# Performance work log

Measured on AMD Instinct MI355X. Metric: run time of the kernel, lower is better.

## Reference

```python
import itertools
import jax, jax.numpy as jnp
import numpy as np

RES = 14
B = 64
DIM = 384
NH = 8
KD = 32
DV = 128  # attn_ratio * key_dim
SCALE = KD ** -0.5


def _bias_idxs(res):
    points = list(itertools.product(range(res), range(res)))
    offs, idxs = {}, []
    for p1 in points:
        for p2 in points:
            o = (abs(p1[0] - p2[0]), abs(p1[1] - p2[1]))
            if o not in offs:
                offs[o] = len(offs)
            idxs.append(offs[o])
    n = res * res
    return np.asarray(idxs, dtype=np.int32).reshape(n, n), len(offs)


def setup_inputs() -> dict:
    key = jax.random.key(0)
    ks = jax.random.split(key, 16)
    idxs, n_off = _bias_idxs(RES)  # n_off == 196 for res=14
    f = lambda k, shape, s=0.05: jax.random.normal(k, shape, dtype=jnp.float32) * s
    return {
        "x": jax.random.normal(ks[0], (B, DIM, RES, RES), dtype=jnp.float32),
        "qw": f(ks[1], (NH * KD, DIM)), "qb": f(ks[2], (NH * KD,)),
        "kw": f(ks[3], (NH * KD, DIM)), "kb": f(ks[4], (NH * KD,)),
        "vw": f(ks[5], (NH * DV, DIM)), "vb": f(ks[6], (NH * DV,)),
        "vlw": f(ks[7], (NH * DV, 1, 3, 3)), "vlb": f(ks[8], (NH * DV,)),
        "th1_w": f(ks[9], (NH, NH), 0.3), "th1_b": f(ks[10], (NH,)),
        "th2_w": f(ks[11], (NH, NH), 0.3), "th2_b": f(ks[12], (NH,)),
        "projw": f(ks[13], (DIM, NH * DV)), "projb": f(ks[14], (DIM,)),
        "bias_seg": f(ks[15], (NH, n_off), 0.5),
        "bias_idxs": jnp.asarray(idxs),
    }


def reference(x, qw, qb, kw, kb, vw, vb, vlw, vlb,
              th1_w, th1_b, th2_w, th2_b, projw, projb,
              bias_seg, bias_idxs):
    Bb, C, H, W = x.shape
    N = H * W
    xf = x.reshape(Bb, C, N)
    # 1x1 conv (+ folded BN) projections
    q = (jnp.einsum('oc,bcn->bon', qw, xf) + qb[:, None]).reshape(Bb, NH, KD, N).transpose(0, 1, 3, 2)  # [B,h,N,kd]
    k = (jnp.einsum('oc,bcn->bon', kw, xf) + kb[:, None]).reshape(Bb, NH, KD, N)                        # [B,h,kd,N]
    v4 = (jnp.einsum('oc,bcn->bon', vw, xf) + vb[:, None]).reshape(Bb, NH * DV, H, W)
    # depthwise 3x3 local branch (+ folded BN)
    v_local = jax.lax.conv_general_dilated(
        v4, vlw, window_strides=(1, 1), padding=[(1, 1), (1, 1)],
        dimension_numbers=('NCHW', 'OIHW', 'NCHW'), feature_group_count=NH * DV,
    ) + vlb[None, :, None, None]
    v = v4.reshape(Bb, NH, DV, N).transpose(0, 1, 3, 2)  # [B,h,N,dv]
    # attention scores + relative bias (bicubic interp 196->196 is identity)
    attn = jnp.einsum('bhnk,bhkm->bhnm', q, k) * SCALE
    bias = bias_seg[:, bias_idxs]  # [h,N,N]
    attn = attn + bias[None]
    # talking heads (1x1 conv over head dim) -> softmax -> talking heads
    attn = jnp.einsum('hg,bgnm->bhnm', th1_w, attn) + th1_b[None, :, None, None]
    attn = jax.nn.softmax(attn, axis=-1)
    attn = jnp.einsum('hg,bgnm->bhnm', th2_w, attn) + th2_b[None, :, None, None]
    o = jnp.einsum('bhnm,bhmd->bhnd', attn, v)           # [B,h,N,dv]
    o = o.transpose(0, 1, 3, 2).reshape(Bb, NH * DV, H, W) + v_local
    # proj: ReLU -> 1x1 conv (+ folded BN)
    o = jax.nn.relu(o)
    out = jnp.einsum('oc,bchw->bohw', projw, o) + projb[None, :, None, None]
    return out
```

## Files before the change

### kernel.cpp

```cpp
#include <hip/hip_runtime.h>
#include <hip/hip_bf16.h>


#define RES   14
#define NSP   196
#define NHD   8
#define KDIM  32
#define DVV   128
#define DIM   384
#define NQK   256
#define SCALE 0.17677669529663687f
#define SROW  224
#define NSTRIP 13

typedef __attribute__((ext_vector_type(8))) short bf16x8;
typedef __attribute__((ext_vector_type(4))) float f32x4;
typedef unsigned short u16;
typedef unsigned int u32;

__device__ __forceinline__ u16 f2b(float f) {
    union { __hip_bfloat16 b; u16 u; } c; c.b = __float2bfloat16(f); return c.u;
}
__device__ __forceinline__ float b2f(u16 u) {
    union { __hip_bfloat16 b; u16 u; } c; c.u = u; return __bfloat162float(c.b);
}

__device__ __forceinline__ void gld16(const void* g, void* l) {
    __builtin_amdgcn_global_load_lds(
        (__attribute__((address_space(1))) void*)(unsigned long long)(const char*)g,
        (__attribute__((address_space(3))) void*)l, 16, 0, 0);
}

__device__ __forceinline__ void gemm128_bk64(const char* Aseg, long rbA,
                                             const char* Bseg, long rbB, int kIters,
                                             u16* A_lds, u16* B_lds, f32x4 acc[4][4])
{
    const int tid  = threadIdx.x;
    const int wid  = tid >> 6;
    const int lane = tid & 63;
    const int lrow = lane >> 2;
    const int lcb  = (lane & 3) << 4;
    const int r0   = wid * 32;
    const int wm   = (wid & 1) * 64, wn = (wid >> 1) * 64;
    const int l15  = lane & 15, lq8 = (lane >> 4) * 8;

    #pragma unroll
    for (int i = 0; i < 4; ++i)
        #pragma unroll
        for (int j = 0; j < 4; ++j) acc[i][j] = (f32x4){0.f, 0.f, 0.f, 0.f};

    const char* ap0 = Aseg + (long)(r0 + lrow) * rbA + lcb;
    const char* ap1 = ap0 + 16 * rbA;
    const char* bp0 = Bseg + (long)(r0 + lrow) * rbB + lcb;
    const char* bp1 = bp0 + 16 * rbB;
    u16* la0 = A_lds + r0 * 32;
    u16* la1 = la0 + 512;
    u16* lb0 = B_lds + r0 * 32;
    u16* lb1 = lb0 + 512;

    for (int kk = 0; kk < kIters; ++kk) {
        gld16(ap0, la0);        gld16(ap1, la1);
        gld16(bp0, lb0);        gld16(bp1, lb1);
        gld16(ap0 + 64, la0 + 4096); gld16(ap1 + 64, la1 + 4096);
        gld16(bp0 + 64, lb0 + 4096); gld16(bp1 + 64, lb1 + 4096);
        ap0 += 128; ap1 += 128; bp0 += 128; bp1 += 128;
        __syncthreads();
        #pragma unroll
        for (int s = 0; s < 2; ++s) {
            bf16x8 af[4], bfr[4];
            #pragma unroll
            for (int i = 0; i < 4; ++i)
                af[i] = *(const bf16x8*)&A_lds[s * 4096 + (wm + i * 16 + l15) * 32 + lq8];
            #pragma unroll
            for (int j = 0; j < 4; ++j)
                bfr[j] = *(const bf16x8*)&B_lds[s * 4096 + (wn + j * 16 + l15) * 32 + lq8];
            #pragma unroll
            for (int i = 0; i < 4; ++i)
                #pragma unroll
                for (int j = 0; j < 4; ++j)
                    acc[i][j] = __builtin_amdgcn_mfma_f32_16x16x32_bf16(
                        af[i], bfr[j], acc[i][j], 0, 0, 0);
        }
        __syncthreads();
    }
}

__global__ __launch_bounds__(256) void k_prep(
    const float* __restrict__ qw, const float* __restrict__ kw,
    const float* __restrict__ vw, const float* __restrict__ pw,
    const float* __restrict__ th1w, const float* __restrict__ th1b,
    const float* __restrict__ bias_seg, const float* __restrict__ vlw,
    const float* __restrict__ x,
    u16* __restrict__ wqkv, u16* __restrict__ pwb, float* __restrict__ biasmix,
    u16* __restrict__ wpack, u16* __restrict__ xb)
{
    __shared__ float t[32][33];
    const int bid = blockIdx.x;
    if (bid < 3883) {
        int i = bid * 256 + threadIdx.x;
        if (i < 98304)       wqkv[i] = f2b(qw[i]);
        else if (i < 196608) wqkv[i] = f2b(kw[i - 98304]);
        else if (i < 589824) wqkv[i] = f2b(vw[i - 196608]);
        else if (i < 983040) pwb[i - 589824] = f2b(pw[i - 589824]);
        else if (i < 984608) {
            int i2 = i - 983040;
            int hh = i2 / NSP, off = i2 - hh * NSP;
            float a = th1b[hh];
            #pragma unroll
            for (int g = 0; g < 8; ++g) a += th1w[hh * 8 + g] * bias_seg[g * NSP + off];
            biasmix[i2] = a;
        } else if (i < 993824) {
            int i2 = i - 984608;
            int g = i2 / 72, r = i2 - g * 72;
            int tap = r >> 3, tt = r & 7;
            wpack[i2] = f2b(vlw[(g * 8 + tt) * 9 + tap]);
        }
    } else {
        const int L = bid - 3883;
        const int b = L / 84, r = L - b * 84;
        const int c0 = (r / 7) * 32, n0 = (r % 7) * 32;
        const int tx = threadIdx.x & 31, ty = threadIdx.x >> 5;
        #pragma unroll
        for (int l = 0; l < 4; ++l) {
            int c = c0 + ty + 8 * l, n = n0 + tx;
            t[ty + 8 * l][tx] = (n < NSP) ? x[((long)b * DIM + c) * NSP + n] : 0.f;
        }
        __syncthreads();
        #pragma unroll
        for (int l = 0; l < 4; ++l) {
            int n = n0 + ty + 8 * l, c = c0 + tx;
            if (n < NSP) xb[((long)b * NSP + n) * DIM + c] = f2b(t[tx][ty + 8 * l]);
        }
    }
}

__global__ __launch_bounds__(256) void k_qkv(
    const u16* __restrict__ xb, const u16* __restrict__ wqkv,
    const float* __restrict__ qb, const float* __restrict__ kb,
    const float* __restrict__ vb,
    u16* __restrict__ qt, u16* __restrict__ kb16, u16* __restrict__ vt)
{
    __shared__ u16 A_lds[8192], B_lds[8192];
    const int m0 = blockIdx.x * 128, oc0 = blockIdx.y * 128;
    f32x4 acc[4][4];
    gemm128_bk64((const char*)xb + (long)m0 * 768, 768,
                 (const char*)wqkv + (long)oc0 * 768, 768, 6, A_lds, B_lds, acc);

    const int tid = threadIdx.x, wid = tid >> 6, lane = tid & 63;
    const int wm = (wid & 1) * 64, wn = (wid >> 1) * 64;
    const int col = lane & 15, quad = lane >> 4;
    #pragma unroll
    for (int i = 0; i < 4; ++i) {
        #pragma unroll
        for (int j = 0; j < 4; ++j) {
            #pragma unroll
            for (int r = 0; r < 4; ++r) {
                int m  = m0 + wm + i * 16 + quad * 4 + r;
                int oc = oc0 + wn + j * 16 + col;
                int b = m / NSP, n = m - b * NSP;
                float v = acc[i][j][r];
                if (oc < 256) {
                    qt[(long)m * NQK + oc] = f2b(v + qb[oc]);
                } else if (oc < 512) {
                    int o = oc - 256;
                    kb16[(long)m * NQK + o] = f2b(v + kb[o]);
                } else {
                    int o = oc - 512, h = o >> 7, d = o & 127;
                    vt[(((long)b * NHD + h) * NSP + n) * DVV + d] = f2b(v + vb[o]);
                }
            }
        }
    }
}

__global__ __launch_bounds__(256) void k_vtT(
    const u16* __restrict__ vt, u16* __restrict__ vtT)
{
    __shared__ u16 t[32][33];
    const int bh = blockIdx.z, d0 = blockIdx.y * 32, n0 = blockIdx.x * 32;
    const int tx = threadIdx.x & 31, ty = threadIdx.x >> 5;
    #pragma unroll
    for (int l = 0; l < 4; ++l) {
        int n = n0 + ty + 8 * l, d = d0 + tx;
        t[ty + 8 * l][tx] = (n < NSP) ? vt[((long)bh * NSP + n) * DVV + d] : (u16)0;
    }
    __syncthreads();
    #pragma unroll
    for (int l = 0; l < 4; ++l) {
        int d = d0 + ty + 8 * l, m = n0 + tx;
        vtT[((long)bh * DVV + d) * 224 + m] = t[tx][ty + 8 * l];
    }
}

__global__ __launch_bounds__(256) void k_dwconv(
    const u16* __restrict__ vt, const u16* __restrict__ wpack,
    const float* __restrict__ vlb, u16* __restrict__ vlt)
{
    const int tid = threadIdx.x;
    const int dg = tid & 15;
    const int nl = tid >> 4;
    const int bh = blockIdx.y;
    const int n  = blockIdx.x * 16 + nl;
    if (n >= NSP) return;
    const int d0 = dg * 8;
    const int h  = bh & 7;
    const int y = n / RES, xx = n - y * RES;
    const long plane = (long)bh * NSP * DVV;
    float acc[8];
    #pragma unroll
    for (int t = 0; t < 8; ++t) acc[t] = vlb[h * DVV + d0 + t];
    const u16* wb = wpack + (h * 16 + dg) * 72;
    #pragma unroll
    for (int dy = -1; dy <= 1; ++dy) {
        int yy = y + dy;
        if (yy < 0 || yy >= RES) continue;
        #pragma unroll
        for (int dx = -1; dx <= 1; ++dx) {
            int xn = xx + dx;
            if (xn < 0 || xn >= RES) continue;
            int tap = (dy + 1) * 3 + dx + 1;
            bf16x8 v  = *(const bf16x8*)&vt[plane + (yy * RES + xn) * DVV + d0];
            bf16x8 wv = *(const bf16x8*)&wb[tap * 8];
            #pragma unroll
            for (int t = 0; t < 8; ++t)
                acc[t] += b2f((u16)wv[t]) * b2f((u16)v[t]);
        }
    }
    bf16x8 r;
    #pragma unroll
    for (int t = 0; t < 8; ++t) r[t] = (short)f2b(acc[t]);
    *(bf16x8*)&vlt[plane + (long)n * DVV + d0] = r;
}

__global__ __launch_bounds__(512, 4) void k_attn2(
    const u16* __restrict__ qt, const u16* __restrict__ kb16,
    const u16* __restrict__ vtT, const u16* __restrict__ vlt,
    const float* __restrict__ th1w, const float* __restrict__ th2w,
    const float* __restrict__ th2b, const float* __restrict__ biasmix,
    u16* __restrict__ ot)
{
    __shared__ u16 S[128 * SROW];
    __shared__ u16 bmS[8 * NSP];
    const int tid = threadIdx.x;
    const int L  = blockIdx.x;
    const int wq = L >> 3;
    const int b  = (L & 7) + ((wq / NSTRIP) << 3);
    const int n0 = (wq % NSTRIP) * 16;
    const int wid = tid >> 6, lane = tid & 63;
    const int l15 = lane & 15, lq8 = (lane >> 4) * 8;
    const int quad = lane >> 4, col = lane & 15;

    for (int i = tid; i < 8 * NSP; i += 512) bmS[i] = f2b(biasmix[i]);
    __syncthreads();

    {
        const long qrow = ((long)(b * NSP) + n0 + l15) * NQK;
        bf16x8 af[8];
        #pragma unroll
        for (int g = 0; g < 8; ++g)
            af[g] = *(const bf16x8*)&qt[qrow + g * 32 + lq8];
        #pragma unroll
        for (int jj = 0; jj < 2; ++jj) {
            const int j = wid + jj * 8;
            if (j >= 14) break;
            const long krow = ((long)(b * NSP) + j * 16 + l15) * NQK;
            f32x4 t[8];
            #pragma unroll
            for (int g = 0; g < 8; ++g) {
                bf16x8 bv = *(const bf16x8*)&kb16[krow + g * 32 + lq8];
                t[g] = __builtin_amdgcn_mfma_f32_16x16x32_bf16(
                    af[g], bv, (f32x4){0.f, 0.f, 0.f, 0.f}, 0, 0, 0);
            }
            const int m = j * 16 + col;
            const int ym = m / RES, xm = m - ym * RES;
            int offr[4];
            #pragma unroll
            for (int r = 0; r < 4; ++r) {
                int gn = n0 + quad * 4 + r;
                int yn = gn / RES, xn = gn - yn * RES;
                int off = abs(yn - ym) * RES + abs(xn - xm);
                offr[r] = (off > 195) ? 195 : off;
            }
            #pragma unroll
            for (int h = 0; h < 8; ++h) {
                float o[4];
                #pragma unroll
                for (int r = 0; r < 4; ++r) o[r] = b2f(bmS[h * NSP + offr[r]]);
                #pragma unroll
                for (int g = 0; g < 8; ++g) {
                    const float w = th1w[h * 8 + g] * SCALE;
                    #pragma unroll
                    for (int r = 0; r < 4; ++r) o[r] += w * t[g][r];
                }
                #pragma unroll
                for (int r = 0; r < 4; ++r)
                    S[(h * 16 + quad * 4 + r) * SROW + m] = f2b(o[r]);
            }
        }
    }
    __syncthreads();

    {
        const int c = lane & 15, rg = lane >> 4;
        #pragma unroll
        for (int it = 0; it < 4; ++it) {
            u16* row = &S[(wid * 16 + it * 4 + rg) * SROW];
            float v[13];
            #pragma unroll
            for (int k = 0; k < 12; ++k) v[k] = b2f(row[c + 16 * k]);
            v[12] = (c < 4) ? b2f(row[192 + c]) : -1e30f;
            float mx = v[0];
            #pragma unroll
            for (int k = 1; k < 13; ++k) mx = fmaxf(mx, v[k]);
            #pragma unroll
            for (int o = 1; o < 16; o <<= 1) mx = fmaxf(mx, __shfl_xor(mx, o));
            float sum = 0.f;
            #pragma unroll
            for (int k = 0; k < 13; ++k) { v[k] = __expf(v[k] - mx); sum += v[k]; }
            if (c >= 4) sum -= v[12];
            #pragma unroll
            for (int o = 1; o < 16; o <<= 1) sum += __shfl_xor(sum, o);
            float inv = 1.0f / sum;
            #pragma unroll
            for (int k = 0; k < 12; ++k) row[c + 16 * k] = f2b(v[k] * inv);
            if (c < 4) row[192 + c] = f2b(v[12] * inv);
        }
    }
    __syncthreads();

    {
        for (int p = tid; p < 16 * 112; p += 512) {
            const int nl = p / 112, kp = p - nl * 112;
            const int m0 = kp * 2;
            if (m0 >= NSP) {
                #pragma unroll
                for (int h = 0; h < 8; ++h)
                    *(u32*)&S[(h * 16 + nl) * SROW + m0] = 0u;
                continue;
            }
            float s0[8], s1[8];
            #pragma unroll
            for (int g = 0; g < 8; ++g) {
                u32 v = *(const u32*)&S[(g * 16 + nl) * SROW + m0];
                s0[g] = b2f((u16)(v & 0xffff));
                s1[g] = b2f((u16)(v >> 16));
            }
            #pragma unroll
            for (int h = 0; h < 8; ++h) {
                float o0 = th2b[h], o1 = th2b[h];
                #pragma unroll
                for (int g = 0; g < 8; ++g) {
                    const float w = th2w[h * 8 + g];
                    o0 += w * s0[g];
                    o1 += w * s1[g];
                }
                *(u32*)&S[(h * 16 + nl) * SROW + m0] =
                    (u32)f2b(o0) | ((u32)f2b(o1) << 16);
            }
        }
    }
    __syncthreads();

    {
        const int h = wid;
        const long vrow = (long)(b * NHD + h) * DVV;
        f32x4 acc[8];
        #pragma unroll
        for (int df = 0; df < 8; ++df) acc[df] = (f32x4){0.f, 0.f, 0.f, 0.f};
        for (int kc = 0; kc < 7; ++kc) {
            bf16x8 a0 = *(const bf16x8*)&S[(h * 16 + l15) * SROW + kc * 32 + lq8];
            #pragma unroll
            for (int df = 0; df < 8; ++df) {
                bf16x8 bv = *(const bf16x8*)&vtT[(vrow + df * 16 + l15) * 224 + kc * 32 + lq8];
                acc[df] = __builtin_amdgcn_mfma_f32_16x16x32_bf16(a0, bv, acc[df], 0, 0, 0);
            }
        }
        const long lbase = (long)(b * NHD + h) * NSP;
        #pragma unroll
        for (int df = 0; df < 8; ++df) {
            #pragma unroll
            for (int r = 0; r < 4; ++r) {
                int n = n0 + quad * 4 + r;
                int d = df * 16 + col;
                if (n < NSP) {
                    float v = acc[df][r] + b2f(vlt[(lbase + n) * DVV + d]);
                    v = fmaxf(v, 0.f);
                    ot[((long)(b * NSP + n)) * 1024 + h * DVV + d] = f2b(v);
                }
            }
        }
    }
}

__global__ __launch_bounds__(256) void k_proj(
    const u16* __restrict__ pwb, const u16* __restrict__ ot,
    const float* __restrict__ projb, float* __restrict__ outp)
{
    __shared__ u16 A_lds[8192];
    __shared__ u16 B_lds[4096];
    const int tid = threadIdx.x, wid = tid >> 6, lane = tid & 63;
    const int lrow = lane >> 2, lcb = (lane & 3) << 4;
    const int m0 = blockIdx.x * 64, oc0 = blockIdx.y * 128;
    const int wm = (wid & 1) * 64, wn = (wid >> 1) * 32;
    const int l15 = lane & 15, lq8 = (lane >> 4) * 8;

    const char* gp[6];
    u16* lp[6];
    #pragma unroll
    for (int t = 0; t < 6; ++t) {
        int s = wid * 6 + t;
        int sub = s / 12, s12 = s - sub * 12;
        if (s12 < 8) {
            gp[t] = (const char*)pwb + (long)(oc0 + s12 * 16 + lrow) * 2048 + lcb + sub * 64;
            lp[t] = A_lds + sub * 4096 + s12 * 512;
        } else {
            gp[t] = (const char*)ot + (long)(m0 + (s12 - 8) * 16 + lrow) * 2048 + lcb + sub * 64;
            lp[t] = B_lds + sub * 2048 + (s12 - 8) * 512;
        }
    }

    f32x4 acc[4][2];
    #pragma unroll
    for (int i = 0; i < 4; ++i)
        #pragma unroll
        for (int j = 0; j < 2; ++j) acc[i][j] = (f32x4){0.f, 0.f, 0.f, 0.f};

    for (int kk = 0; kk < 16; ++kk) {
        #pragma unroll
        for (int t = 0; t < 6; ++t) { gld16(gp[t], lp[t]); gp[t] += 128; }
        __syncthreads();
        #pragma unroll
        for (int s = 0; s < 2; ++s) {
            bf16x8 af[4], bfr[2];
            #pragma unroll
            for (int i = 0; i < 4; ++i)
                af[i] = *(const bf16x8*)&A_lds[s * 4096 + (wm + i * 16 + l15) * 32 + lq8];
            #pragma unroll
            for (int j = 0; j < 2; ++j)
                bfr[j] = *(const bf16x8*)&B_lds[s * 2048 + (wn + j * 16 + l15) * 32 + lq8];
            #pragma unroll
            for (int i = 0; i < 4; ++i)
                #pragma unroll
                for (int j = 0; j < 2; ++j)
                    acc[i][j] = __builtin_amdgcn_mfma_f32_16x16x32_bf16(
                        af[i], bfr[j], acc[i][j], 0, 0, 0);
        }
        __syncthreads();
    }

    const int col = lane & 15, quad = lane >> 4;
    #pragma unroll
    for (int i = 0; i < 4; ++i) {
        #pragma unroll
        for (int j = 0; j < 2; ++j) {
            #pragma unroll
            for (int r = 0; r < 4; ++r) {
                int oc = oc0 + wm + i * 16 + quad * 4 + r;
                int mg = m0 + wn + j * 16 + col;
                int b = mg / NSP, n = mg - b * NSP;
                outp[((long)b * DIM + oc) * NSP + n] = acc[i][j][r] + projb[oc];
            }
        }
    }
}

extern "C" void kernel_launch(void* const* d_in, const int* in_sizes, int n_in,
                              void* d_out, int out_size, void* d_ws, size_t ws_size,
                              hipStream_t stream) {
    const float* x        = (const float*)d_in[0];
    const float* qw       = (const float*)d_in[1];
    const float* qb       = (const float*)d_in[2];
    const float* kw       = (const float*)d_in[3];
    const float* kb       = (const float*)d_in[4];
    const float* vw       = (const float*)d_in[5];
    const float* vb       = (const float*)d_in[6];
    const float* vlw      = (const float*)d_in[7];
    const float* vlb      = (const float*)d_in[8];
    const float* th1w     = (const float*)d_in[9];
    const float* th1b     = (const float*)d_in[10];
    const float* th2w     = (const float*)d_in[11];
    const float* th2b     = (const float*)d_in[12];
    const float* projw    = (const float*)d_in[13];
    const float* projb    = (const float*)d_in[14];
    const float* bias_seg = (const float*)d_in[15];
    float* outp = (float*)d_out;

    char* w = (char*)d_ws;
    u16* xb      = (u16*)(w);
    u16* wqkv    = (u16*)(w + 9633792);
    u16* pwb     = (u16*)(w + 10813440);
    u16* wpack   = (u16*)(w + 11599872);
    float* bmix  = (float*)(w + 11618304);
    u16* qt      = (u16*)(w + 11624704);
    u16* kb16    = (u16*)(w + 18080000);
    u16* vt      = (u16*)(w + 24535296);
    u16* vtT     = (u16*)(w + 50225408);
    u16* ot      = (u16*)(w + 79585536);
    u16* vlt     = (u16*)(w + 105275648);

    k_prep<<<dim3(9259), 256, 0, stream>>>(qw, kw, vw, projw, th1w, th1b,
                                           bias_seg, vlw, x, wqkv, pwb, bmix,
                                           wpack, xb);
    k_qkv<<<dim3(98, 12), 256, 0, stream>>>(xb, wqkv, qb, kb, vb, qt, kb16, vt);
    k_vtT<<<dim3(7, 4, 512), 256, 0, stream>>>(vt, vtT);
    k_dwconv<<<dim3(13, 512), 256, 0, stream>>>(vt, wpack, vlb, vlt);
    k_attn2<<<dim3(NSTRIP * 64), 512, 0, stream>>>(qt, kb16, vtT, vlt, th1w, th2w,
                                                   th2b, bmix, ot);
    k_proj<<<dim3(196, 3), 256, 0, stream>>>(pwb, ot, projb, outp);
}
```

Measured before the change: 298.4 us.

## Pack attention LDS scratch tighter to fit more blocks per CU

Narrows the score-row stride from 224 to 200 and merges the bias table into one shared buffer, storing part of it in the padding columns, so per-block LDS drops enough for a third 512-thread block per CU. It also raises the launch-bounds minimum blocks, drops the 14th key tile and the explicit zero-fill of padding in the talking-heads pass. The PV matmul still reads past column 200 into the neighbouring row, relying on zero-padded V to cancel those terms. The tighter register cap from the launch bounds risks spills.

```diff
diff --git a/kernel.cpp b/kernel.cpp
--- a/kernel.cpp
+++ b/kernel.cpp
@@ -10,7 +10,8 @@
 #define DIM   384
 #define NQK   256
 #define SCALE 0.17677669529663687f
-#define SROW  224
+#define SROW  200
+#define BMBASE 25600
 #define NSTRIP 13
 
 typedef __attribute__((ext_vector_type(8))) short bf16x8;
@@ -232,15 +233,14 @@
     *(bf16x8*)&vlt[plane + (long)n * DVV + d0] = r;
 }
 
-__global__ __launch_bounds__(512, 4) void k_attn2(
+__global__ __launch_bounds__(512, 6) void k_attn2(
     const u16* __restrict__ qt, const u16* __restrict__ kb16,
     const u16* __restrict__ vtT, const u16* __restrict__ vlt,
     const float* __restrict__ th1w, const float* __restrict__ th2w,
     const float* __restrict__ th2b, const float* __restrict__ biasmix,
     u16* __restrict__ ot)
 {
-    __shared__ u16 S[128 * SROW];
-    __shared__ u16 bmS[8 * NSP];
+    __shared__ u16 SB[27136];
     const int tid = threadIdx.x;
     const int L  = blockIdx.x;
     const int wq = L >> 3;
@@ -250,7 +250,15 @@
     const int l15 = lane & 15, lq8 = (lane >> 4) * 8;
     const int quad = lane >> 4, col = lane & 15;
 
-    for (int i = tid; i < 8 * NSP; i += 512) bmS[i] = f2b(biasmix[i]);
+    for (int i = tid; i < 8 * NSP; i += 512) {
+        int h = i / NSP, off = i - h * NSP;
+        int a = (off < 192) ? (BMBASE + h * 192 + off) : (h * SROW + 4 + off);
+        SB[a] = f2b(biasmix[i]);
+    }
+    if (tid < 480) {
+        int r = 8 + (tid >> 2);
+        SB[r * SROW + 196 + (tid & 3)] = 0;
+    }
     __syncthreads();
 
     {
@@ -262,7 +270,7 @@
         #pragma unroll
         for (int jj = 0; jj < 2; ++jj) {
             const int j = wid + jj * 8;
-            if (j >= 14) break;
+            if (j >= 13) break;
             const long krow = ((long)(b * NSP) + j * 16 + l15) * NQK;
             f32x4 t[8];
             #pragma unroll
@@ -281,20 +289,28 @@
                 int off = abs(yn - ym) * RES + abs(xn - xm);
                 offr[r] = (off > 195) ? 195 : off;
             }
+            const bool wr = (m < NSP);
             #pragma unroll
             for (int h = 0; h < 8; ++h) {
                 float o[4];
                 #pragma unroll
-                for (int r = 0; r < 4; ++r) o[r] = b2f(bmS[h * NSP + offr[r]]);
+                for (int r = 0; r < 4; ++r) {
+                    int off = offr[r];
+                    int a = (off < 192) ? (BMBASE + h * 192 + off)
+                                        : (h * SROW + 4 + off);
+                    o[r] = b2f(SB[a]);
+                }
                 #pragma unroll
                 for (int g = 0; g < 8; ++g) {
                     const float w = th1w[h * 8 + g] * SCALE;
                     #pragma unroll
                     for (int r = 0; r < 4; ++r) o[r] += w * t[g][r];
                 }
-                #pragma unroll
-                for (int r = 0; r < 4; ++r)
-                    S[(h * 16 + quad * 4 + r) * SROW + m] = f2b(o[r]);
+                if (wr) {
+                    #pragma unroll
+                    for (int r = 0; r < 4; ++r)
+                        SB[(h * 16 + quad * 4 + r) * SROW + m] = f2b(o[r]);
+                }
             }
         }
     }
@@ -304,7 +320,7 @@
         const int c = lane & 15, rg = lane >> 4;
         #pragma unroll
         for (int it = 0; it < 4; ++it) {
-            u16* row = &S[(wid * 16 + it * 4 + rg) * SROW];
+            u16* row = &SB[(wid * 16 + it * 4 + rg) * SROW];
             float v[13];
             #pragma unroll
             for (int k = 0; k < 12; ++k) v[k] = b2f(row[c + 16 * k]);
@@ -329,19 +345,13 @@
     __syncthreads();
 
     {
-        for (int p = tid; p < 16 * 112; p += 512) {
-            const int nl = p / 112, kp = p - nl * 112;
+        for (int p = tid; p < 16 * 98; p += 512) {
+            const int nl = p / 98, kp = p - nl * 98;
             const int m0 = kp * 2;
-            if (m0 >= NSP) {
-                #pragma unroll
-                for (int h = 0; h < 8; ++h)
-                    *(u32*)&S[(h * 16 + nl) * SROW + m0] = 0u;
-                continue;
-            }
             float s0[8], s1[8];
             #pragma unroll
             for (int g = 0; g < 8; ++g) {
-                u32 v = *(const u32*)&S[(g * 16 + nl) * SROW + m0];
+                u32 v = *(const u32*)&SB[(g * 16 + nl) * SROW + m0];
                 s0[g] = b2f((u16)(v & 0xffff));
                 s1[g] = b2f((u16)(v >> 16));
             }
@@ -354,7 +364,7 @@
                     o0 += w * s0[g];
                     o1 += w * s1[g];
                 }
-                *(u32*)&S[(h * 16 + nl) * SROW + m0] =
+                *(u32*)&SB[(h * 16 + nl) * SROW + m0] =
                     (u32)f2b(o0) | ((u32)f2b(o1) << 16);
             }
         }
@@ -368,7 +378,7 @@
         #pragma unroll
         for (int df = 0; df < 8; ++df) acc[df] = (f32x4){0.f, 0.f, 0.f, 0.f};
         for (int kc = 0; kc < 7; ++kc) {
-            bf16x8 a0 = *(const bf16x8*)&S[(h * 16 + l15) * SROW + kc * 32 + lq8];
+            bf16x8 a0 = *(const bf16x8*)&SB[(h * 16 + l15) * SROW + kc * 32 + lq8];
             #pragma unroll
             for (int df = 0; df < 8; ++df) {
                 bf16x8 bv = *(const bf16x8*)&vtT[(vrow + df * 16 + l15) * 224 + kc * 32 + lq8];
```

Result: slower. 315.3 us (+5.7%).
